# Kernel optimization log

Measured on AMD Instinct MI355X. Metric: run time of the kernel, lower is better.

Reference implementation:

```python
import jax, jax.numpy as jnp
import numpy as np

B, T, C, H = 4, 2048, 1024, 16
HS = C // H  # 64
THRESH_INIT = (5 + 1) / 12 * 0.01  # (layer_idx+1)/n_layer * final_token_threshold


def _layernorm(x, w, b, eps=1e-5):
    mu = jnp.mean(x, axis=-1, keepdims=True)
    var = jnp.var(x, axis=-1, keepdims=True)
    return (x - mu) * jax.lax.rsqrt(var + eps) * w + b


def setup_inputs() -> dict:
    key = jax.random.key(0)
    ks = jax.random.split(key, 8)
    s = 0.02
    inp = {
        'x': jax.random.normal(ks[0], (B, T, C), dtype=jnp.float32),
        'attention_mask': jnp.ones((B, T), dtype=jnp.float32),
        'protected_mask': jnp.zeros((B, T), dtype=jnp.float32),
        'ln1_w': jnp.ones((C,), jnp.float32),
        'ln1_b': jnp.zeros((C,), jnp.float32),
        'c_attn_w': jax.random.normal(ks[1], (3 * C, C), jnp.float32) * s,
        'c_attn_b': jnp.zeros((3 * C,), jnp.float32),
        'c_proj_w': jax.random.normal(ks[2], (C, C), jnp.float32) * s,
        'c_proj_b': jnp.zeros((C,), jnp.float32),
        'ln2_w': jnp.ones((C,), jnp.float32),
        'ln2_b': jnp.zeros((C,), jnp.float32),
        'fc_w': jax.random.normal(ks[3], (4 * C, C), jnp.float32) * s,
        'fc_b': jnp.zeros((4 * C,), jnp.float32),
        'fcproj_w': jax.random.normal(ks[4], (C, 4 * C), jnp.float32) * s,
        'fcproj_b': jnp.zeros((C,), jnp.float32),
        'threshold': jnp.asarray(THRESH_INIT, jnp.float32),
    }
    return inp


def reference(x, attention_mask, protected_mask, ln1_w, ln1_b, c_attn_w, c_attn_b,
              c_proj_w, c_proj_b, ln2_w, ln2_b, fc_w, fc_b, fcproj_w, fcproj_b, threshold):
    b, t, c = x.shape
    # --- attention with importance scores ---
    h = _layernorm(x, ln1_w, ln1_b)
    qkv = h @ c_attn_w.T + c_attn_b                      # (B,T,3C)
    q, k, v = jnp.split(qkv, 3, axis=-1)
    q = q.reshape(b, t, H, HS).transpose(0, 2, 1, 3)     # (B,H,T,hs)
    k = k.reshape(b, t, H, HS).transpose(0, 2, 1, 3)
    v = v.reshape(b, t, H, HS).transpose(0, 2, 1, 3)
    att = jnp.einsum('bhqd,bhkd->bhqk', q, k) / np.sqrt(HS)
    causal = jnp.tril(jnp.ones((t, t), dtype=bool))      # (T,T)
    att = jnp.where(causal[None, None], att, -jnp.inf)
    att = jnp.where(attention_mask[:, None, None, :] != 0, att, -jnp.inf)
    att = jax.nn.softmax(att, axis=-1)                   # (B,H,T,T)
    y = jnp.einsum('bhqk,bhkd->bhqd', att, v)
    y = y.transpose(0, 2, 1, 3).reshape(b, t, c)
    y = y @ c_proj_w.T + c_proj_b
    importance = att.mean(axis=1).mean(axis=1)           # (B,T): mean over heads, then queries
    # --- pruning ---
    x = x + y
    pruning_mask = (importance >= threshold).astype(x.dtype)  # hard mode
    pruning_mask = jnp.where(protected_mask > 0, jnp.ones_like(pruning_mask), pruning_mask)
    combined_mask = attention_mask * pruning_mask
    x = x * combined_mask[..., None]
    # --- MLP ---
    m = _layernorm(x, ln2_w, ln2_b)
    m = jax.nn.gelu(m @ fc_w.T + fc_b, approximate=False)
    x = x + (m @ fcproj_w.T + fcproj_b)
    pruning_loss = jnp.asarray(0.0, x.dtype)  # hard mode / lambda=0
    return (x, combined_mask, pruning_loss)
```

## Files before the change

### kernel.cpp

```cpp
#include <hip/hip_runtime.h>
#include <math.h>

#define B_ 4
#define T_ 2048
#define C_ 1024
#define H_ 16
#define NROWS (B_*T_)

typedef short s8v  __attribute__((ext_vector_type(8)));
typedef float f4v  __attribute__((ext_vector_type(4)));
typedef unsigned short u16v4 __attribute__((ext_vector_type(4)));

#define QSCALE 0.1803368801111f

static __device__ __forceinline__ unsigned short f2bf(float x) {
    unsigned u = __float_as_uint(x);
    unsigned r = u + 0x7fffu + ((u >> 16) & 1u);
    return (unsigned short)(r >> 16);
}

static __device__ __forceinline__ float fexp2(float x) {
    return __builtin_amdgcn_exp2f(x);
}

static __device__ __forceinline__ void gload_lds16(const void* g, void* l) {
    __builtin_amdgcn_global_load_lds(
        (const __attribute__((address_space(1))) void*)g,
        (__attribute__((address_space(3))) void*)l, 16, 0, 0);
}

__global__ __launch_bounds__(256) void prep_kernel(
        const float* __restrict__ x, const float* __restrict__ w,
        const float* __restrict__ b, unsigned short* __restrict__ out,
        const float* __restrict__ wsrc, unsigned short* __restrict__ wdst,
        float* __restrict__ imp, int* __restrict__ nsurv)
{
    int row = blockIdx.x;
    int tid = threadIdx.x;
    int widx = row * 96 + tid;
    if (tid < 96) {
        float4 v = ((const float4*)wsrc)[widx];
        u16v4 o = { f2bf(v.x), f2bf(v.y), f2bf(v.z), f2bf(v.w) };
        *(u16v4*)(wdst + (size_t)widx*4) = o;
    }
    if (row < 32) imp[row*256 + tid] = 0.f;
    if (row == 32 && tid < 8) nsurv[tid] = 0;

    const float4* xr = (const float4*)(x + (size_t)row * C_);
    float4 v = xr[tid];
    float s  = v.x + v.y + v.z + v.w;
    float ss = v.x*v.x + v.y*v.y + v.z*v.z + v.w*v.w;
    #pragma unroll
    for (int off = 32; off > 0; off >>= 1) {
        s  += __shfl_down(s,  off, 64);
        ss += __shfl_down(ss, off, 64);
    }
    __shared__ float rs[4], rss[4];
    __shared__ float smu, srstd;
    int wave = tid >> 6, lane = tid & 63;
    if (lane == 0) { rs[wave] = s; rss[wave] = ss; }
    __syncthreads();
    if (tid == 0) {
        float S  = rs[0]+rs[1]+rs[2]+rs[3];
        float SS = rss[0]+rss[1]+rss[2]+rss[3];
        float mu = S * (1.0f/C_);
        float var = SS * (1.0f/C_) - mu*mu;
        smu = mu; srstd = rsqrtf(var + 1e-5f);
    }
    __syncthreads();
    float mu = smu, rstd = srstd;
    float4 wv = ((const float4*)w)[tid];
    float4 bv = ((const float4*)b)[tid];
    u16v4 o;
    o.x = f2bf((v.x-mu)*rstd*wv.x + bv.x);
    o.y = f2bf((v.y-mu)*rstd*wv.y + bv.y);
    o.z = f2bf((v.z-mu)*rstd*wv.z + bv.z);
    o.w = f2bf((v.w-mu)*rstd*wv.w + bv.w);
    *(u16v4*)(out + (size_t)row * C_ + tid*4) = o;
}

__global__ __launch_bounds__(256) void ln_bf16(const float* __restrict__ x,
        const float* __restrict__ w, const float* __restrict__ b,
        unsigned short* __restrict__ out, const int* __restrict__ flag, int nrows)
{
    if (flag && flag[0] == 0) return;
    int tid = threadIdx.x;
    __shared__ float rs[4], rss[4];
    __shared__ float smu, srstd;
    int wave = tid >> 6, lane = tid & 63;
    for (int row = blockIdx.x; row < nrows; row += gridDim.x) {
        const float4* xr = (const float4*)(x + (size_t)row * C_);
        float4 v = xr[tid];
        float s  = v.x + v.y + v.z + v.w;
        float ss = v.x*v.x + v.y*v.y + v.z*v.z + v.w*v.w;
        #pragma unroll
        for (int off = 32; off > 0; off >>= 1) {
            s  += __shfl_down(s,  off, 64);
            ss += __shfl_down(ss, off, 64);
        }
        if (lane == 0) { rs[wave] = s; rss[wave] = ss; }
        __syncthreads();
        if (tid == 0) {
            float S  = rs[0]+rs[1]+rs[2]+rs[3];
            float SS = rss[0]+rss[1]+rss[2]+rss[3];
            float mu = S * (1.0f/C_);
            float var = SS * (1.0f/C_) - mu*mu;
            smu = mu; srstd = rsqrtf(var + 1e-5f);
        }
        __syncthreads();
        float mu = smu, rstd = srstd;
        float4 wv = ((const float4*)w)[tid];
        float4 bv = ((const float4*)b)[tid];
        u16v4 o;
        o.x = f2bf((v.x-mu)*rstd*wv.x + bv.x);
        o.y = f2bf((v.y-mu)*rstd*wv.y + bv.y);
        o.z = f2bf((v.z-mu)*rstd*wv.z + bv.z);
        o.w = f2bf((v.w-mu)*rstd*wv.w + bv.w);
        *(u16v4*)(out + (size_t)row * C_ + tid*4) = o;
        __syncthreads();
    }
}

__global__ __launch_bounds__(256) void cvt3_bf16(
        const float* __restrict__ cprojw, const float* __restrict__ fcw,
        const float* __restrict__ fcpw,
        unsigned short* __restrict__ wproj, unsigned short* __restrict__ wfc,
        unsigned short* __restrict__ wfcp, const int* __restrict__ flag)
{
    if (flag[0] == 0) return;
    const int total = 9*C_*C_/4;
    const int n1 = C_*C_/4;
    const int n2 = n1 + C_*C_;
    for (int i = blockIdx.x * 256 + threadIdx.x; i < total; i += gridDim.x * 256) {
        const float* src; unsigned short* dst; int j;
        if (i < n1)      { src = cprojw; dst = wproj; j = i; }
        else if (i < n2) { src = fcw;    dst = wfc;   j = i - n1; }
        else             { src = fcpw;   dst = wfcp;  j = i - n2; }
        float4 v = ((const float4*)src)[j];
        u16v4 o = { f2bf(v.x), f2bf(v.y), f2bf(v.z), f2bf(v.w) };
        *(u16v4*)(dst + (size_t)j*4) = o;
    }
}

template<int EPI>
__global__ __launch_bounds__(256) void gemm_bf16(
    const unsigned short* __restrict__ A,
    const unsigned short* __restrict__ Bw,
    const float* __restrict__ bias,
    const float* __restrict__ res,
    float* __restrict__ Cout, unsigned short* __restrict__ Cbf,
    int K, int lda, int ldb, int ldc, int ncoff,
    const float* __restrict__ cmv,
    unsigned short* __restrict__ qh, unsigned short* __restrict__ kh,
    unsigned short* __restrict__ vh, const int* __restrict__ flag,
    int nbx, int nby)
{
    if (flag && flag[0] == 0) return;
    __shared__ unsigned short As[128*64];
    __shared__ unsigned short Bs[128*64];
    int tid = threadIdx.x;
    int w = tid >> 6, lane = tid & 63, quad = lane >> 4, l16 = lane & 15;
    int wr = w >> 1, wc = w & 1;

    int nvb = nbx * nby;
    int vb0 = blockIdx.y * gridDim.x + blockIdx.x;
    int vstride = gridDim.x * gridDim.y;

    for (int vb = vb0; vb < nvb; vb += vstride) {
        int n0 = (vb % nbx) * 128;
        int m0 = (vb / nbx) * 128;

        size_t offA[4], offB[4];
        #pragma unroll
        for (int j = 0; j < 4; j++) {
            int ci = j*256 + tid;
            int mr = ci >> 3, kcs = ci & 7;
            int kc = kcs ^ (mr & 7);
            offA[j] = (size_t)(m0 + mr) * lda + kc*8;
            offB[j] = (size_t)(n0 + mr) * ldb + kc*8;
        }

        f4v acc[4][4];
        #pragma unroll
        for (int i = 0; i < 4; i++)
            #pragma unroll
            for (int j = 0; j < 4; j++) { acc[i][j][0]=0.f; acc[i][j][1]=0.f; acc[i][j][2]=0.f; acc[i][j][3]=0.f; }

        for (int k0 = 0; k0 < K; k0 += 64) {
            __syncthreads();
            #pragma unroll
            for (int j = 0; j < 4; j++) {
                gload_lds16(A  + offA[j] + k0, &As[(j*256 + (w<<6))*8]);
                gload_lds16(Bw + offB[j] + k0, &Bs[(j*256 + (w<<6))*8]);
            }
            __syncthreads();
            #pragma unroll
            for (int c = 0; c < 2; c++) {
                s8v af[4], bf[4];
                int sw = ((c<<2) + quad) ^ (l16 & 7);
                #pragma unroll
                for (int i = 0; i < 4; i++) {
                    int mr = wr*64 + i*16 + l16;
                    af[i] = *(const s8v*)&As[mr*64 + sw*8];
                    int nr = wc*64 + i*16 + l16;
                    bf[i] = *(const s8v*)&Bs[nr*64 + sw*8];
                }
                #pragma unroll
                for (int i = 0; i < 4; i++)
                    #pragma unroll
                    for (int j = 0; j < 4; j++)
                        acc[i][j] = __builtin_amdgcn_mfma_f32_16x16x32_bf16(af[i], bf[j], acc[i][j], 0, 0, 0);
            }
        }

        #pragma unroll
        for (int j = 0; j < 4; j++) {
            int ncol = n0 + wc*64 + j*16 + l16;
            float bv = bias ? bias[ncol] : 0.f;
            int hh = 0, dd = 0;
            bool qsec = false;
            unsigned short* basep = nullptr;
            if (EPI == 3) {
                int ncolg = ncol + ncoff;
                int sec = ncolg >> 10;
                int hn = ncolg & 1023;
                hh = hn >> 6; dd = hn & 63;
                basep = (sec == 0) ? qh : (sec == 1) ? kh : vh;
                qsec = (sec == 0);
            }
            #pragma unroll
            for (int i = 0; i < 4; i++) {
                #pragma unroll
                for (int reg = 0; reg < 4; reg++) {
                    int m = m0 + wr*64 + i*16 + quad*4 + reg;
                    float v = acc[i][j][reg] + bv;
                    if (EPI == 1) {
                        v = 0.5f * v * (1.0f + erff(v * 0.70710678118654752f));
                        Cbf[(size_t)m*ldc + ncol] = f2bf(v);
                    } else if (EPI == 2) {
                        Cout[(size_t)m*ldc + ncol] = v + res[(size_t)m*ldc + ncol];
                    } else if (EPI == 3) {
                        if (qsec) v *= QSCALE;
                        int bb = m >> 11, t = m & 2047;
                        basep[(((size_t)(bb*H_ + hh))*T_ + t)*64 + dd] = f2bf(v);
                    } else if (EPI == 4) {
                        Cout[(size_t)m*ldc + ncol] = (res[(size_t)m*ldc + ncol] + v) * cmv[m];
                    }
                }
            }
        }
    }
}

__global__ __launch_bounds__(256) void attn_rowsum(
    const unsigned short* __restrict__ qh, const unsigned short* __restrict__ kh,
    const float* __restrict__ amask, float* __restrict__ linvbuf)
{
    __shared__ float msk01[2048];
    __shared__ float lred[4][64];

    int tid = threadIdx.x;
    int w = tid >> 6, lane = tid & 63, quad = lane >> 4, l16 = lane & 15;
    int qt = 31 - (blockIdx.x >> 6);
    int bh = blockIdx.x & 63;
    int b  = bh >> 4;
    int q0 = qt * 64;
    int ntiles = qt + 1;

    const unsigned short* qp = qh + (size_t)bh*T_*64;
    const unsigned short* kp = kh + (size_t)bh*T_*64;
    const float* amp = amask + b*T_;

    for (int i = tid; i < ntiles*64; i += 256)
        msk01[i] = (amp[i] != 0.f) ? 1.f : 0.f;
    __syncthreads();

    s8v aQ[4][2];
    #pragma unroll
    for (int qf = 0; qf < 4; qf++) {
        int row = q0 + qf*16 + l16;
        aQ[qf][0] = *(const s8v*)(qp + (size_t)row*64 + quad*8);
        aQ[qf][1] = *(const s8v*)(qp + (size_t)row*64 + 32 + quad*8);
    }

    float lrow[4][4];
    #pragma unroll
    for (int qf = 0; qf < 4; qf++)
        #pragma unroll
        for (int reg = 0; reg < 4; reg++) lrow[qf][reg] = 0.f;

    for (int it = w; it < ntiles; it += 4) {
        int k0 = it * 64;
        s8v bk[2][4];
        #pragma unroll
        for (int c = 0; c < 2; c++)
            #pragma unroll
            for (int nt = 0; nt < 4; nt++)
                bk[c][nt] = *(const s8v*)(kp + (size_t)(k0 + nt*16 + l16)*64 + c*32 + quad*8);
        float mk[4];
        #pragma unroll
        for (int nt = 0; nt < 4; nt++) mk[nt] = msk01[k0 + nt*16 + l16];
        bool allm = __all(mk[0] != 0.f && mk[1] != 0.f && mk[2] != 0.f && mk[3] != 0.f);

        #pragma unroll
        for (int qf = 0; qf < 4; qf++) {
            f4v acc[4];
            #pragma unroll
            for (int nt = 0; nt < 4; nt++) { acc[nt][0]=0.f; acc[nt][1]=0.f; acc[nt][2]=0.f; acc[nt][3]=0.f; }
            #pragma unroll
            for (int c = 0; c < 2; c++)
                #pragma unroll
                for (int nt = 0; nt < 4; nt++)
                    acc[nt] = __builtin_amdgcn_mfma_f32_16x16x32_bf16(aQ[qf][c], bk[c][nt], acc[nt], 0, 0, 0);
            if (it < qt && allm) {
                #pragma unroll
                for (int nt = 0; nt < 4; nt++)
                    #pragma unroll
                    for (int reg = 0; reg < 4; reg++)
                        lrow[qf][reg] += fexp2(acc[nt][reg]);
            } else if (it < qt) {
                #pragma unroll
                for (int nt = 0; nt < 4; nt++)
                    #pragma unroll
                    for (int reg = 0; reg < 4; reg++)
                        lrow[qf][reg] += fexp2(acc[nt][reg]) * mk[nt];
            } else {
                #pragma unroll
                for (int nt = 0; nt < 4; nt++) {
                    int kg = k0 + nt*16 + l16;
                    #pragma unroll
                    for (int reg = 0; reg < 4; reg++) {
                        float me = (kg <= q0 + qf*16 + quad*4 + reg) ? mk[nt] : 0.f;
                        lrow[qf][reg] += fexp2(acc[nt][reg]) * me;
                    }
                }
            }
        }
    }

    #pragma unroll
    for (int qf = 0; qf < 4; qf++)
        #pragma unroll
        for (int reg = 0; reg < 4; reg++) {
            float v = lrow[qf][reg];
            v += __shfl_xor(v, 1); v += __shfl_xor(v, 2);
            v += __shfl_xor(v, 4); v += __shfl_xor(v, 8);
            lrow[qf][reg] = v;
        }
    if (l16 == 0) {
        #pragma unroll
        for (int qf = 0; qf < 4; qf++)
            #pragma unroll
            for (int reg = 0; reg < 4; reg++)
                lred[w][qf*16 + quad*4 + reg] = lrow[qf][reg];
    }
    __syncthreads();
    if (tid < 64) {
        float t = lred[0][tid] + lred[1][tid] + lred[2][tid] + lred[3][tid];
        linvbuf[(size_t)bh*T_ + q0 + tid] = (t > 0.f) ? 1.0f / t : 0.f;
    }
}

__global__ __launch_bounds__(256) void attn_colsum(
    const unsigned short* __restrict__ qh, const unsigned short* __restrict__ kh,
    const float* __restrict__ amask, const float* __restrict__ linvbuf,
    float* __restrict__ imp)
{
    __shared__ float cred[4][64];

    int tid = threadIdx.x;
    int w = tid >> 6, lane = tid & 63, quad = lane >> 4, l16 = lane & 15;
    int kc = blockIdx.x >> 6;
    int bh = blockIdx.x & 63;
    int b  = bh >> 4;
    int k0 = kc * 64;

    const unsigned short* qp = qh + (size_t)bh*T_*64;
    const unsigned short* kp = kh + (size_t)bh*T_*64;
    const float* lp = linvbuf + (size_t)bh*T_;

    s8v bk[2][4];
    float mk[4];
    #pragma unroll
    for (int nt = 0; nt < 4; nt++) {
        int key = k0 + nt*16 + l16;
        bk[0][nt] = *(const s8v*)(kp + (size_t)key*64 + quad*8);
        bk[1][nt] = *(const s8v*)(kp + (size_t)key*64 + 32 + quad*8);
        mk[nt] = amask[b*T_ + key];
    }

    float cs[4] = {0.f, 0.f, 0.f, 0.f};

    for (int qt = kc + w; qt < 32; qt += 4) {
        int q0 = qt * 64;
        #pragma unroll
        for (int qf = 0; qf < 4; qf++) {
            int row = q0 + qf*16 + l16;
            s8v a0 = *(const s8v*)(qp + (size_t)row*64 + quad*8);
            s8v a1 = *(const s8v*)(qp + (size_t)row*64 + 32 + quad*8);
            float4 linv4 = *(const float4*)(lp + q0 + qf*16 + quad*4);
            f4v acc[4];
            #pragma unroll
            for (int nt = 0; nt < 4; nt++) { acc[nt][0]=0.f; acc[nt][1]=0.f; acc[nt][2]=0.f; acc[nt][3]=0.f; }
            #pragma unroll
            for (int nt = 0; nt < 4; nt++) {
                acc[nt] = __builtin_amdgcn_mfma_f32_16x16x32_bf16(a0, bk[0][nt], acc[nt], 0, 0, 0);
                acc[nt] = __builtin_amdgcn_mfma_f32_16x16x32_bf16(a1, bk[1][nt], acc[nt], 0, 0, 0);
            }
            float lv[4] = { linv4.x, linv4.y, linv4.z, linv4.w };
            if (qt > kc) {
                #pragma unroll
                for (int nt = 0; nt < 4; nt++)
                    #pragma unroll
                    for (int reg = 0; reg < 4; reg++)
                        cs[nt] += fexp2(acc[nt][reg]) * lv[reg];
            } else {
                #pragma unroll
                for (int nt = 0; nt < 4; nt++) {
                    int kg = k0 + nt*16 + l16;
                    #pragma unroll
                    for (int reg = 0; reg < 4; reg++) {
                        float me = (kg <= q0 + qf*16 + quad*4 + reg) ? 1.f : 0.f;
                        cs[nt] += fexp2(acc[nt][reg]) * lv[reg] * me;
                    }
                }
            }
        }
    }

    #pragma unroll
    for (int nt = 0; nt < 4; nt++) {
        float v = cs[nt] * mk[nt];
        v += __shfl_xor(v, 16);
        v += __shfl_xor(v, 32);
        if (quad == 0) cred[w][nt*16 + l16] = v;
    }
    __syncthreads();
    if (tid < 64)
        atomicAdd(&imp[b*T_ + k0 + tid],
                  cred[0][tid] + cred[1][tid] + cred[2][tid] + cred[3][tid]);
}

__global__ __launch_bounds__(256) void mask_finalize(
    const float* __restrict__ imp, const float* __restrict__ amask,
    const float* __restrict__ prot, const float* __restrict__ thr,
    float* __restrict__ mask_out, float* __restrict__ loss_out,
    int* __restrict__ nsurv)
{
    int i = blockIdx.x * 256 + threadIdx.x;
    float impv = imp[i] * (1.0f / (float)(H_ * T_));
    float pm = (impv >= thr[0]) ? 1.f : 0.f;
    if (prot[i] > 0.f) pm = 1.f;
    float cm = amask[i] * pm;
    mask_out[i] = cm;
    if (i == 0) loss_out[0] = 0.f;
    unsigned long long bal = __ballot(cm != 0.f);
    int cnt = __popcll(bal);
    __shared__ int bs;
    if (threadIdx.x == 0) bs = 0;
    __syncthreads();
    if ((threadIdx.x & 63) == 0 && cnt) atomicAdd(&bs, cnt);
    __syncthreads();
    if (threadIdx.x == 0 && bs) atomicAdd(nsurv, bs);
}

__global__ __launch_bounds__(256) void attn_full(
    const unsigned short* __restrict__ qh, const unsigned short* __restrict__ kh,
    const unsigned short* __restrict__ vh, const float* __restrict__ amask,
    unsigned short* __restrict__ y, const int* __restrict__ flag)
{
    if (flag[0] == 0) return;
    __shared__ unsigned short Ks[64][72];
    __shared__ unsigned short Vt[64][72];
    __shared__ unsigned short Ps[4][16][72];
    __shared__ float mks[64];

    int tid = threadIdx.x;
    int w = tid >> 6, lane = tid & 63, quad = lane >> 4, l16 = lane & 15;
    int nqt = T_ / 64;

    for (int vb = blockIdx.x; vb < B_*H_*nqt; vb += gridDim.x) {
        int qt = vb % nqt;
        int bh = vb / nqt;
        int b = bh >> 4, h = bh & 15;
        int q0 = qt * 64;

        const unsigned short* qp = qh + (size_t)bh * T_ * 64;
        const unsigned short* kp = kh + (size_t)bh * T_ * 64;
        const unsigned short* vp = vh + (size_t)bh * T_ * 64;

        int qrow = q0 + 16*w + l16;
        s8v aQ0 = *(const s8v*)(qp + (size_t)qrow*64 + quad*8);
        s8v aQ1 = *(const s8v*)(qp + (size_t)qrow*64 + 32 + quad*8);

        int qwmax = q0 + 16*w + 15;
        int ntiles = qt + 1;
        int qg = q0 + 16*w + quad*4;

        float lrow[4] = {0.f, 0.f, 0.f, 0.f};
        for (int it = 0; it < ntiles; ++it) {
            int k0 = it * 64;
            __syncthreads();
            for (int cid = tid; cid < 512; cid += 256) {
                int row = cid >> 3, ch = cid & 7;
                *(s8v*)&Ks[row][ch*8] = *(const s8v*)(kp + (size_t)(k0+row)*64 + ch*8);
            }
            if (tid < 64) mks[tid] = amask[b*T_ + k0 + tid];
            __syncthreads();
            if (k0 > qwmax) continue;
            f4v accS[4];
            #pragma unroll
            for (int nt = 0; nt < 4; nt++) { accS[nt][0]=0.f; accS[nt][1]=0.f; accS[nt][2]=0.f; accS[nt][3]=0.f; }
            #pragma unroll
            for (int nt = 0; nt < 4; nt++) {
                s8v b0 = *(const s8v*)&Ks[nt*16 + l16][quad*8];
                s8v b1 = *(const s8v*)&Ks[nt*16 + l16][32 + quad*8];
                accS[nt] = __builtin_amdgcn_mfma_f32_16x16x32_bf16(aQ0, b0, accS[nt], 0, 0, 0);
                accS[nt] = __builtin_amdgcn_mfma_f32_16x16x32_bf16(aQ1, b1, accS[nt], 0, 0, 0);
            }
            #pragma unroll
            for (int nt = 0; nt < 4; nt++) {
                int kg = k0 + nt*16 + l16;
                float mkv = mks[nt*16 + l16];
                #pragma unroll
                for (int reg = 0; reg < 4; reg++) {
                    bool val = (kg <= qg + reg) && (mkv != 0.f);
                    float e = fexp2(accS[nt][reg]);
                    lrow[reg] += val ? e : 0.f;
                }
            }
        }
        float linv[4];
        #pragma unroll
        for (int reg = 0; reg < 4; reg++) {
            float v = lrow[reg];
            v += __shfl_xor(v, 1); v += __shfl_xor(v, 2);
            v += __shfl_xor(v, 4); v += __shfl_xor(v, 8);
            linv[reg] = (v > 0.f) ? 1.0f / v : 0.f;
        }

        f4v accO[4];
        #pragma unroll
        for (int nt = 0; nt < 4; nt++) { accO[nt][0]=0.f; accO[nt][1]=0.f; accO[nt][2]=0.f; accO[nt][3]=0.f; }

        for (int it = 0; it < ntiles; ++it) {
            int k0 = it * 64;
            __syncthreads();
            for (int cid = tid; cid < 512; cid += 256) {
                int row = cid >> 3, ch = cid & 7;
                s8v kv = *(const s8v*)(kp + (size_t)(k0+row)*64 + ch*8);
                *(s8v*)&Ks[row][ch*8] = kv;
                s8v vv = *(const s8v*)(vp + (size_t)(k0+row)*64 + ch*8);
                #pragma unroll
                for (int j = 0; j < 8; j++) Vt[ch*8 + j][row] = (unsigned short)vv[j];
            }
            if (tid < 64) mks[tid] = amask[b*T_ + k0 + tid];
            __syncthreads();
            if (k0 > qwmax) continue;
            f4v accS[4];
            #pragma unroll
            for (int nt = 0; nt < 4; nt++) { accS[nt][0]=0.f; accS[nt][1]=0.f; accS[nt][2]=0.f; accS[nt][3]=0.f; }
            #pragma unroll
            for (int nt = 0; nt < 4; nt++) {
                s8v b0 = *(const s8v*)&Ks[nt*16 + l16][quad*8];
                s8v b1 = *(const s8v*)&Ks[nt*16 + l16][32 + quad*8];
                accS[nt] = __builtin_amdgcn_mfma_f32_16x16x32_bf16(aQ0, b0, accS[nt], 0, 0, 0);
                accS[nt] = __builtin_amdgcn_mfma_f32_16x16x32_bf16(aQ1, b1, accS[nt], 0, 0, 0);
            }
            #pragma unroll
            for (int nt = 0; nt < 4; nt++) {
                int kg = k0 + nt*16 + l16;
                float mkv = mks[nt*16 + l16];
                #pragma unroll
                for (int reg = 0; reg < 4; reg++) {
                    bool val = (kg <= qg + reg) && (mkv != 0.f);
                    float p = val ? fexp2(accS[nt][reg]) * linv[reg] : 0.f;
                    Ps[w][quad*4 + reg][nt*16 + l16] = f2bf(p);
                }
            }
            s8v aP0 = *(const s8v*)&Ps[w][l16][quad*8];
            s8v aP1 = *(const s8v*)&Ps[w][l16][32 + quad*8];
            #pragma unroll
            for (int nt = 0; nt < 4; nt++) {
                s8v bv0 = *(const s8v*)&Vt[nt*16 + l16][quad*8];
                s8v bv1 = *(const s8v*)&Vt[nt*16 + l16][32 + quad*8];
                accO[nt] = __builtin_amdgcn_mfma_f32_16x16x32_bf16(aP0, bv0, accO[nt], 0, 0, 0);
                accO[nt] = __builtin_amdgcn_mfma_f32_16x16x32_bf16(aP1, bv1, accO[nt], 0, 0, 0);
            }
        }
        #pragma unroll
        for (int nt = 0; nt < 4; nt++) {
            #pragma unroll
            for (int reg = 0; reg < 4; reg++) {
                int q = q0 + 16*w + quad*4 + reg;
                y[((size_t)(b*T_ + q))*C_ + h*64 + nt*16 + l16] = f2bf(accO[nt][reg]);
            }
        }
        __syncthreads();
    }
}

__global__ __launch_bounds__(256) void ap_fc(const int* __restrict__ nsurv,
        const float* __restrict__ ln2b, const float* __restrict__ fcw,
        const float* __restrict__ fcb, float* __restrict__ abuf)
{
    if (nsurv[0] != 0) return;
    int j = blockIdx.x * 4 + (threadIdx.x >> 6);
    int lane = threadIdx.x & 63;
    const float4* wr = (const float4*)(fcw + (size_t)j * C_);
    const float4* bb = (const float4*)ln2b;
    float s = 0.f;
    #pragma unroll
    for (int k = 0; k < 4; k++) {
        float4 a = bb[lane + 64*k];
        float4 wv = wr[lane + 64*k];
        s += a.x*wv.x + a.y*wv.y + a.z*wv.z + a.w*wv.w;
    }
    #pragma unroll
    for (int off = 32; off > 0; off >>= 1) s += __shfl_down(s, off, 64);
    if (lane == 0) {
        float v = fcb[j] + s;
        abuf[j] = 0.5f * v * (1.0f + erff(v * 0.70710678118654752f));
    }
}

__global__ __launch_bounds__(256) void ap_fcp(const int* __restrict__ nsurv,
        const float* __restrict__ abuf, const float* __restrict__ fcpw,
        const float* __restrict__ fcpb, float* __restrict__ rowbuf)
{
    if (nsurv[0] != 0) return;
    int c = blockIdx.x * 4 + (threadIdx.x >> 6);
    int lane = threadIdx.x & 63;
    const float4* wr = (const float4*)(fcpw + (size_t)c * (4*C_));
    const float4* ab = (const float4*)abuf;
    float s = 0.f;
    #pragma unroll
    for (int k = 0; k < 16; k++) {
        float4 a = ab[lane + 64*k];
        float4 wv = wr[lane + 64*k];
        s += a.x*wv.x + a.y*wv.y + a.z*wv.z + a.w*wv.w;
    }
    #pragma unroll
    for (int off = 32; off > 0; off >>= 1) s += __shfl_down(s, off, 64);
    if (lane == 0) rowbuf[c] = fcpb[c] + s;
}

__global__ __launch_bounds__(256) void ap_bcast(const int* __restrict__ nsurv,
        const float* __restrict__ rowbuf, float* __restrict__ out_x)
{
    if (nsurv[0] != 0) return;
    float4 v = ((const float4*)rowbuf)[threadIdx.x];
    for (int r = blockIdx.x; r < NROWS; r += gridDim.x)
        ((float4*)(out_x + (size_t)r * C_))[threadIdx.x] = v;
}

extern "C" void kernel_launch(void* const* d_in, const int* in_sizes, int n_in,
                              void* d_out, int out_size, void* d_ws, size_t ws_size,
                              hipStream_t stream) {
    const float* x       = (const float*)d_in[0];
    const float* amask   = (const float*)d_in[1];
    const float* prot    = (const float*)d_in[2];
    const float* ln1w    = (const float*)d_in[3];
    const float* ln1b    = (const float*)d_in[4];
    const float* cattn_w = (const float*)d_in[5];
    const float* cattn_b = (const float*)d_in[6];
    const float* cproj_w = (const float*)d_in[7];
    const float* cproj_b = (const float*)d_in[8];
    const float* ln2w    = (const float*)d_in[9];
    const float* ln2b    = (const float*)d_in[10];
    const float* fcw     = (const float*)d_in[11];
    const float* fcb     = (const float*)d_in[12];
    const float* fcpw    = (const float*)d_in[13];
    const float* fcpb    = (const float*)d_in[14];
    const float* thr     = (const float*)d_in[15];

    unsigned short* wqkv  = (unsigned short*)d_ws;
    unsigned short* wproj = wqkv  + (size_t)3*C_*C_;
    unsigned short* wfc   = wproj + (size_t)C_*C_;
    unsigned short* wfcp  = wfc   + (size_t)4*C_*C_;
    unsigned short* hbuf  = wfcp  + (size_t)4*C_*C_;
    unsigned short* qh    = hbuf  + (size_t)NROWS*C_;
    unsigned short* kh    = qh    + (size_t)NROWS*C_;
    unsigned short* vh    = kh    + (size_t)NROWS*C_;
    unsigned short* cbuf  = qh;
    float* imp    = (float*)(vh + (size_t)NROWS*C_);
    int*   nsurv  = (int*)(imp + NROWS);
    float* abuf   = (float*)(nsurv + 8);
    float* rowbuf = abuf + 4*C_;
    float* linvbuf = rowbuf + C_;

    float* out_x    = (float*)d_out;
    float* out_mask = out_x + (size_t)NROWS*C_;
    float* out_loss = out_mask + NROWS;

    hipLaunchKernelGGL(prep_kernel, dim3(NROWS), dim3(256), 0, stream,
                       x, ln1w, ln1b, hbuf, cattn_w, wqkv, imp, nsurv);
    hipLaunchKernelGGL((gemm_bf16<3>), dim3(16, 64), dim3(256), 0, stream,
                       hbuf, wqkv, cattn_b, nullptr, nullptr, nullptr,
                       C_, C_, C_, 0, 0, nullptr, qh, kh, vh, nullptr, 16, 64);
    hipLaunchKernelGGL(attn_rowsum, dim3(64*32), dim3(256), 0, stream,
                       qh, kh, amask, linvbuf);
    hipLaunchKernelGGL(attn_colsum, dim3(64*32), dim3(256), 0, stream,
                       qh, kh, amask, linvbuf, imp);
    hipLaunchKernelGGL(mask_finalize, dim3(NROWS/256), dim3(256), 0, stream,
                       imp, amask, prot, thr, out_mask, out_loss, nsurv);

    hipLaunchKernelGGL(cvt3_bf16, dim3(512), dim3(256), 0, stream,
                       cproj_w, fcw, fcpw, wproj, wfc, wfcp, nsurv);
    hipLaunchKernelGGL((gemm_bf16<3>), dim3(512), dim3(256), 0, stream,
                       hbuf, wqkv + (size_t)2048*C_, cattn_b + 2048, nullptr, nullptr, nullptr,
                       C_, C_, C_, 0, 2048, nullptr, qh, kh, vh, nsurv, 8, 64);
    hipLaunchKernelGGL(attn_full, dim3(512), dim3(256), 0, stream,
                       qh, kh, vh, amask, hbuf, nsurv);
    hipLaunchKernelGGL((gemm_bf16<4>), dim3(512), dim3(256), 0, stream,
                       hbuf, wproj, cproj_b, x, out_x, nullptr,
                       C_, C_, C_, C_, 0, out_mask, nullptr, nullptr, nullptr, nsurv, 8, 64);
    hipLaunchKernelGGL(ln_bf16, dim3(512), dim3(256), 0, stream,
                       out_x, ln2w, ln2b, hbuf, nsurv, NROWS);
    for (int j = 0; j < 2; j++) {
        hipLaunchKernelGGL((gemm_bf16<1>), dim3(512), dim3(256), 0, stream,
                           hbuf, wfc + (size_t)j*2048*C_, fcb + j*2048, nullptr, nullptr, cbuf,
                           C_, C_, C_, 2048, 0, nullptr, nullptr, nullptr, nullptr, nsurv, 16, 64);
        hipLaunchKernelGGL((gemm_bf16<2>), dim3(512), dim3(256), 0, stream,
                           cbuf, wfcp + (size_t)j*2048, (j == 0) ? fcpb : nullptr, out_x, out_x, nullptr,
                           2048, 2048, 4*C_, C_, 0, nullptr, nullptr, nullptr, nullptr, nsurv, 8, 64);
    }

    hipLaunchKernelGGL(ap_fc,    dim3(4*C_/4), dim3(256), 0, stream, nsurv, ln2b, fcw, fcb, abuf);
    hipLaunchKernelGGL(ap_fcp,   dim3(C_/4),   dim3(256), 0, stream, nsurv, abuf, fcpw, fcpb, rowbuf);
    hipLaunchKernelGGL(ap_bcast, dim3(512),    dim3(256), 0, stream, nsurv, rowbuf, out_x);
}
```

Measured before the change: 313.0 us.

## Add 256x256-tile 8-wave pipelined GEMM for the Q/K projection

Replaces the generic 128-tile bf16 GEMM used for the Q and K projection with a dedicated kernel. It uses 512 threads, 256x256 output tiles and double-buffered LDS filled by direct global-to-LDS loads. Each K-step is split into four sub-phases that interleave the next tiles' loads with MFMA work, and it uses explicit waitcnt/barrier control, setprio and a swizzled block order. The aim is to hide global-load latency and raise MFMA utilisation, at the cost of heavy LDS use (two blocks per CU at most) and fragile hand-written synchronisation.

Measured after the change: 311.8 us. Within noise of the previous version (-0.4%).

```diff
diff --git a/kernel.cpp b/kernel.cpp
--- a/kernel.cpp
+++ b/kernel.cpp
@@ -139,6 +139,122 @@
         float4 v = ((const float4*)src)[j];
         u16v4 o = { f2bf(v.x), f2bf(v.y), f2bf(v.z), f2bf(v.w) };
         *(u16v4*)(dst + (size_t)j*4) = o;
+    }
+}
+
+#define STG(gbase_, ldsarr_, ah_, kt_, bb_) do { \
+    gload_lds16(gbase_ + (size_t)((ah_)*128)*1024 + (kt_)*64, \
+                &ldsarr_[bb_][(((ah_)*128) + (w<<3))*64]); \
+    gload_lds16(gbase_ + (size_t)((ah_)*128 + 64)*1024 + (kt_)*64, \
+                &ldsarr_[bb_][(((ah_)*128 + 64) + (w<<3))*64]); \
+} while (0)
+
+#define PHASE(ah_, bh_, ...) do { \
+    s8v af[4][2], bf[2][2]; \
+    _Pragma("unroll") \
+    for (int i2 = 0; i2 < 4; i2++) { \
+        int arow = ((ah_)*128 + wr*64 + i2*16 + l16)*64; \
+        af[i2][0] = *(const s8v*)&As[bb][arow + (((quad)     ^ (l16&7))<<3)]; \
+        af[i2][1] = *(const s8v*)&As[bb][arow + (((4 + quad) ^ (l16&7))<<3)]; \
+    } \
+    _Pragma("unroll") \
+    for (int j2 = 0; j2 < 2; j2++) { \
+        int brow = ((bh_)*128 + wc*32 + j2*16 + l16)*64; \
+        bf[j2][0] = *(const s8v*)&Bs[bb][brow + (((quad)     ^ (l16&7))<<3)]; \
+        bf[j2][1] = *(const s8v*)&Bs[bb][brow + (((4 + quad) ^ (l16&7))<<3)]; \
+    } \
+    __VA_ARGS__; \
+    asm volatile("s_barrier" ::: "memory"); \
+    asm volatile("s_waitcnt lgkmcnt(0)" ::: "memory"); \
+    __builtin_amdgcn_sched_barrier(0); \
+    __builtin_amdgcn_s_setprio(1); \
+    _Pragma("unroll") \
+    for (int i2 = 0; i2 < 4; i2++) \
+        _Pragma("unroll") \
+        for (int j2 = 0; j2 < 2; j2++) { \
+            acc[(ah_)*4+i2][(bh_)*2+j2] = __builtin_amdgcn_mfma_f32_16x16x32_bf16( \
+                af[i2][0], bf[j2][0], acc[(ah_)*4+i2][(bh_)*2+j2], 0, 0, 0); \
+            acc[(ah_)*4+i2][(bh_)*2+j2] = __builtin_amdgcn_mfma_f32_16x16x32_bf16( \
+                af[i2][1], bf[j2][1], acc[(ah_)*4+i2][(bh_)*2+j2], 0, 0, 0); \
+        } \
+    __builtin_amdgcn_s_setprio(0); \
+    __builtin_amdgcn_sched_barrier(0); \
+    asm volatile("s_barrier" ::: "memory"); \
+} while (0)
+
+__global__ __launch_bounds__(512, 2) void gemm_qk_8ph(
+    const unsigned short* __restrict__ A,
+    const unsigned short* __restrict__ Bw,
+    const float* __restrict__ bias,
+    unsigned short* __restrict__ qh, unsigned short* __restrict__ kh)
+{
+    __shared__ unsigned short As[2][256*64];
+    __shared__ unsigned short Bs[2][256*64];
+
+    const int tid  = threadIdx.x;
+    const int w    = tid >> 6, lane = tid & 63;
+    const int quad = lane >> 4, l16 = lane & 15;
+    const int wr   = w >> 2, wc = w & 3;
+    const int rl   = tid >> 3;
+    const int kc   = (tid & 7) ^ (rl & 7);
+
+    const int bid = blockIdx.x;
+    const int vb  = (bid & 7) * 32 + (bid >> 3);
+    const int m0  = (vb >> 3) << 8;
+    const int n0  = (vb & 7) << 8;
+
+    const unsigned short* gA0 = A  + (size_t)(m0 + rl) * 1024 + kc * 8;
+    const unsigned short* gB0 = Bw + (size_t)(n0 + rl) * 1024 + kc * 8;
+
+    STG(gA0, As, 0, 0, 0);
+    STG(gB0, Bs, 1, 0, 0);
+    STG(gA0, As, 1, 0, 0);
+    STG(gB0, Bs, 0, 0, 0);
+    STG(gA0, As, 0, 1, 1);
+    STG(gB0, Bs, 1, 1, 1);
+
+    f4v acc[8][4];
+    #pragma unroll
+    for (int i = 0; i < 8; i++)
+        #pragma unroll
+        for (int j = 0; j < 4; j++) {
+            acc[i][j][0] = 0.f; acc[i][j][1] = 0.f;
+            acc[i][j][2] = 0.f; acc[i][j][3] = 0.f;
+        }
+
+    #pragma unroll 2
+    for (int t = 0; t < 16; ++t) {
+        const int bb = t & 1, nb = bb ^ 1;
+        if (t < 15) asm volatile("s_waitcnt vmcnt(4)" ::: "memory");
+        else        asm volatile("s_waitcnt vmcnt(0)" ::: "memory");
+        asm volatile("s_barrier" ::: "memory");
+        __builtin_amdgcn_sched_barrier(0);
+        PHASE(0, 0, if (t < 15) STG(gA0, As, 1, t+1, nb));
+        PHASE(0, 1, if (t < 15) STG(gB0, Bs, 0, t+1, nb));
+        PHASE(1, 1, if (t < 14) STG(gA0, As, 0, t+2, bb));
+        PHASE(1, 0, if (t < 14) STG(gB0, Bs, 1, t+2, bb));
+    }
+
+    #pragma unroll
+    for (int j = 0; j < 4; j++) {
+        int ncol = n0 + ((j >> 1) << 7) + (wc << 5) + ((j & 1) << 4) + l16;
+        float bv = bias[ncol];
+        int sec = ncol >> 10;
+        int hh = (ncol & 1023) >> 6, dd = ncol & 63;
+        unsigned short* basep = (sec == 0) ? qh : kh;
+        bool qsec = (sec == 0);
+        #pragma unroll
+        for (int i = 0; i < 8; i++) {
+            int mbase = m0 + ((i >> 2) << 7) + (wr << 6) + ((i & 3) << 4) + (quad << 2);
+            #pragma unroll
+            for (int reg = 0; reg < 4; reg++) {
+                int m = mbase + reg;
+                float v = acc[i][j][reg] + bv;
+                if (qsec) v *= QSCALE;
+                int b_ = m >> 11, tt = m & 2047;
+                basep[(((size_t)(b_*H_ + hh))*T_ + tt)*64 + dd] = f2bf(v);
+            }
+        }
     }
 }
 
@@ -695,9 +811,8 @@
 
     hipLaunchKernelGGL(prep_kernel, dim3(NROWS), dim3(256), 0, stream,
                        x, ln1w, ln1b, hbuf, cattn_w, wqkv, imp, nsurv);
-    hipLaunchKernelGGL((gemm_bf16<3>), dim3(16, 64), dim3(256), 0, stream,
-                       hbuf, wqkv, cattn_b, nullptr, nullptr, nullptr,
-                       C_, C_, C_, 0, 0, nullptr, qh, kh, vh, nullptr, 16, 64);
+    hipLaunchKernelGGL(gemm_qk_8ph, dim3(256), dim3(512), 0, stream,
+                       hbuf, wqkv, cattn_b, qh, kh);
     hipLaunchKernelGGL(attn_rowsum, dim3(64*32), dim3(256), 0, stream,
                        qh, kh, amask, linvbuf);
     hipLaunchKernelGGL(attn_colsum, dim3(64*32), dim3(256), 0, stream,
```
